# Optimization experiments

Hardware: AMD Instinct MI355X
Metric: run time of the kernel (lower is better)

The kernel has to match this reference:

```python
import jax, jax.numpy as jnp
import numpy as np

B, A, G = 256, 64, 978          # batch, n_atoms, num_gene
D_DRUG, D_CELL, D_DOSE = 128, 50, 128
CELL_IN, DOSE_IN = 978, 12
GLOBAL = D_DRUG + D_CELL + D_DOSE   # 306
EXP_IN = GLOBAL + 128               # 434
E, TOP_K = 4, 2


def setup_inputs() -> dict:
    key = jax.random.key(0)
    ks = jax.random.split(key, 24)
    w = lambda k, s: jax.random.normal(k, s, jnp.float32) * 0.05
    return {
        "drug_atom_embed": jax.random.normal(ks[0], (B, A, D_DRUG), jnp.float32),
        "input_cell_gex": jax.random.normal(ks[1], (B, CELL_IN), jnp.float32),
        "input_pert_idose": jax.random.normal(ks[2], (B, DOSE_IN), jnp.float32),
        # LinearEncoder: 978 -> 200 -> 100 -> 50 (ReLU after each)
        "cell_W1": w(ks[3], (CELL_IN, 200)), "cell_b1": jnp.zeros((200,), jnp.float32),
        "cell_W2": w(ks[4], (200, 100)),     "cell_b2": jnp.zeros((100,), jnp.float32),
        "cell_W3": w(ks[5], (100, D_CELL)),  "cell_b3": jnp.zeros((D_CELL,), jnp.float32),
        # DoseEncoder: 12 -> 64 -> 128 (ReLU after each; dropout off at eval)
        "dose_W1": w(ks[6], (DOSE_IN, 64)),  "dose_b1": jnp.zeros((64,), jnp.float32),
        "dose_W2": w(ks[7], (64, D_DOSE)),   "dose_b2": jnp.zeros((D_DOSE,), jnp.float32),
        # gene index embedding [num_gene, 128]
        "gene_emb": w(ks[8], (G, 128)),
        # GatingNetwork: 306 -> 128 -> 4
        "gate_W1": w(ks[9], (GLOBAL, 128)),  "gate_b1": jnp.zeros((128,), jnp.float32),
        "gate_W2": w(ks[10], (128, E)),      "gate_b2": jnp.zeros((E,), jnp.float32),
        # 4 ExpertNetworks stacked: 434 -> 128 -> 1
        "exp_W1": w(ks[11], (E, EXP_IN, 128)), "exp_b1": jnp.zeros((E, 128), jnp.float32),
        "exp_W2": w(ks[12], (E, 128, 1)),      "exp_b2": jnp.zeros((E, 1), jnp.float32),
    }


def reference(drug_atom_embed, input_cell_gex, input_pert_idose,
              cell_W1, cell_b1, cell_W2, cell_b2, cell_W3, cell_b3,
              dose_W1, dose_b1, dose_W2, dose_b2, gene_emb,
              gate_W1, gate_b1, gate_W2, gate_b2,
              exp_W1, exp_b1, exp_W2, exp_b2):
    relu = jax.nn.relu
    # drug: sum atom embeddings -> [B, 128]
    drug = drug_atom_embed.sum(axis=1)
    # cell encoder -> [B, 50]
    cell = relu(input_cell_gex @ cell_W1 + cell_b1)
    cell = relu(cell @ cell_W2 + cell_b2)
    cell = relu(cell @ cell_W3 + cell_b3)
    # dose encoder -> [B, 128]
    dose = relu(input_pert_idose @ dose_W1 + dose_b1)
    dose = relu(dose @ dose_W2 + dose_b2)
    # global features [B, 306]
    g = jnp.concatenate([drug, cell, dose], axis=1)
    # gating: top-k sparse gates [B, E]
    logits = relu(g @ gate_W1 + gate_b1) @ gate_W2 + gate_b2
    top_v, top_i = jax.lax.top_k(logits, TOP_K)
    top_g = jax.nn.softmax(top_v, axis=1)
    gates = jnp.zeros_like(logits).at[jnp.arange(logits.shape[0])[:, None], top_i].set(top_g)
    # gene-aware expert input [B, G, 434]
    expert_input = jnp.concatenate([
        jnp.broadcast_to(g[:, None, :], (g.shape[0], G, GLOBAL)),
        jnp.broadcast_to(gene_emb[None, :, :], (g.shape[0], G, 128)),
    ], axis=2)
    # all experts: [B, E, G, 128] -> [B, E, G]
    h = relu(jnp.einsum('bgi,eih->begh', expert_input, exp_W1) + exp_b1[None, :, None, :])
    o = jnp.einsum('begh,eho->beg', h, exp_W2) + exp_b2[None, :, :1]  # exp_b2[e,0] broadcast
    predictions = jnp.einsum('beg,be->bg', o, gates)
    return predictions, cell
```

## Files before the change

### kernel.cpp

```cpp
#include <hip/hip_runtime.h>

#define NB 256
#define NA 64
#define NG 978
#define CELL_IN 978
#define DOSE_IN 12
#define GLOBAL_F 306
#define EXP_IN 434
#define NE 4

#define WS_SEL 0
#define WS_U   (WS_SEL + NB*4)
#define WS_V   (WS_U + NB*256)

#define A_BLOCKS 256
#define AB_GRID  (NB + A_BLOCKS)

__device__ __forceinline__ float wave_reduce(float p) {
    #pragma unroll
    for (int off = 32; off > 0; off >>= 1) p += __shfl_down(p, off, 64);
    return p;
}

__global__ __launch_bounds__(1024) void ab_kernel(
    const float* __restrict__ drug, const float* __restrict__ gex,
    const float* __restrict__ idose,
    const float* __restrict__ cW1, const float* __restrict__ cb1,
    const float* __restrict__ cW2, const float* __restrict__ cb2,
    const float* __restrict__ cW3, const float* __restrict__ cb3,
    const float* __restrict__ dW1, const float* __restrict__ db1,
    const float* __restrict__ dW2, const float* __restrict__ db2,
    const float* __restrict__ gW1, const float* __restrict__ gb1,
    const float* __restrict__ gW2, const float* __restrict__ gb2,
    const float* __restrict__ eW1, const float* __restrict__ eb1,
    const float* __restrict__ gene,
    float* __restrict__ ws, float* __restrict__ cell_out)
{
    __shared__ float s_gex[CELL_IN];
    __shared__ float s_g[GLOBAL_F];
    __shared__ float s_h1[200];
    __shared__ float s_h2[100];
    __shared__ float s_gh[128];
    __shared__ float s_d1[64];
    __shared__ int   s_isel[2];
    __shared__ float s_part[16 * 200];
    __shared__ float s_pu[32 * 128];
    __shared__ float s_gene[64 * 129];

    const int blk = blockIdx.x, tid = threadIdx.x;

    if (blk >= NB) {
        const int ablk = blk - NB;
        const int tile = ablk >> 4, e = (ablk >> 2) & 3, hq = ablk & 3;

        for (int i = tid; i < 64 * 128; i += 1024) {
            int gl = i >> 7, k = i & 127;
            int g = tile * 64 + gl;
            s_gene[gl * 129 + k] = (g < NG) ? gene[g * 128 + k] : 0.f;
        }
        __syncthreads();

        const int slice = tid >> 6, g_in = tid & 63;
        const int h0 = hq * 32 + slice * 2;
        const float* wbase = eW1 + ((size_t)e * EXP_IN + GLOBAL_F) * 128 + h0;
        float a0 = 0.f, a1 = 0.f;
        #pragma unroll 8
        for (int k = 0; k < 128; ++k) {
            float x = s_gene[g_in * 129 + k];
            float2 w = *(const float2*)(wbase + (size_t)k * 128);
            a0 += x * w.x; a1 += x * w.y;
        }
        float* vout = ws + WS_V + ((size_t)tile * 512 + e * 128 + h0) * 64 + g_in;
        vout[0]  = a0;
        vout[64] = a1;
        return;
    }

    const int b = blk;

    if (tid < CELL_IN) s_gex[tid] = gex[b * CELL_IN + tid];
    {
        int row = tid >> 7, d = tid & 127;
        const float* p = drug + ((size_t)b * NA) * 128 + d;
        float acc = 0.f;
        #pragma unroll
        for (int i = 0; i < 8; ++i) acc += p[(size_t)(i * 8 + row) * 128];
        s_pu[row * 128 + d] = acc;
    }
    __syncthreads();
    if (tid < 128) {
        float a = 0.f;
        #pragma unroll
        for (int r = 0; r < 8; ++r) a += s_pu[r * 128 + tid];
        s_g[tid] = a;
    } else if (tid < 192) {
        int j = tid - 128;
        float acc = db1[j];
        #pragma unroll
        for (int i = 0; i < DOSE_IN; ++i)
            acc += idose[b * DOSE_IN + i] * dW1[i * 64 + j];
        s_d1[j] = fmaxf(acc, 0.f);
    }
    __syncthreads();
    if (tid < 128) {
        float acc = db2[tid];
        #pragma unroll 8
        for (int i = 0; i < 64; ++i) acc += s_d1[i] * dW2[i * 128 + tid];
        s_g[178 + tid] = fmaxf(acc, 0.f);
    }
    __syncthreads();

    {
        int q = tid & 63, ks = tid >> 6;
        if (q < 50) {
            int i0 = ks * 62, i1 = min(i0 + 62, CELL_IN);
            float4 acc = {0.f, 0.f, 0.f, 0.f};
            #pragma unroll 4
            for (int i = i0; i < i1; ++i) {
                float4 w = *(const float4*)(cW1 + (size_t)i * 200 + 4 * q);
                float x = s_gex[i];
                acc.x += x * w.x; acc.y += x * w.y; acc.z += x * w.z; acc.w += x * w.w;
            }
            *(float4*)(&s_part[ks * 200 + 4 * q]) = acc;
        }
    }
    __syncthreads();
    if (tid < 200) {
        float a = cb1[tid];
        #pragma unroll
        for (int ks = 0; ks < 16; ++ks) a += s_part[ks * 200 + tid];
        s_h1[tid] = fmaxf(a, 0.f);
    }
    __syncthreads();

    {
        int q = tid & 31, ks = tid >> 5;
        if (q < 25 && ks < 16) {
            int i0 = ks * 13, i1 = min(i0 + 13, 200);
            float4 acc = {0.f, 0.f, 0.f, 0.f};
            #pragma unroll
            for (int i = i0; i < i1; ++i) {
                float4 w = *(const float4*)(cW2 + (size_t)i * 100 + 4 * q);
                float x = s_h1[i];
                acc.x += x * w.x; acc.y += x * w.y; acc.z += x * w.z; acc.w += x * w.w;
            }
            *(float4*)(&s_part[ks * 100 + 4 * q]) = acc;
        }
    }
    __syncthreads();
    if (tid < 100) {
        float a = cb2[tid];
        #pragma unroll
        for (int ks = 0; ks < 16; ++ks) a += s_part[ks * 100 + tid];
        s_h2[tid] = fmaxf(a, 0.f);
    }
    __syncthreads();

    {
        int j = tid & 63, ks = tid >> 6;
        if (j < 50 && ks < 8) {
            int i0 = ks * 13, i1 = min(i0 + 13, 100);
            float acc = 0.f;
            #pragma unroll
            for (int i = i0; i < i1; ++i) acc += s_h2[i] * cW3[i * 50 + j];
            s_part[ks * 64 + j] = acc;
        }
    }
    __syncthreads();
    if (tid < 50) {
        float a = cb3[tid];
        #pragma unroll
        for (int ks = 0; ks < 8; ++ks) a += s_part[ks * 64 + tid];
        float r = fmaxf(a, 0.f);
        s_g[128 + tid] = r;
        cell_out[b * 50 + tid] = r;
    }
    __syncthreads();

    {
        int q = tid & 31, ks = tid >> 5;
        if (ks < 16) {
            int i0 = ks * 20, i1 = min(i0 + 20, GLOBAL_F);
            float4 acc = {0.f, 0.f, 0.f, 0.f};
            #pragma unroll
            for (int i = i0; i < i1; ++i) {
                float4 w = *(const float4*)(gW1 + (size_t)i * 128 + 4 * q);
                float x = s_g[i];
                acc.x += x * w.x; acc.y += x * w.y; acc.z += x * w.z; acc.w += x * w.w;
            }
            *(float4*)(&s_part[ks * 128 + 4 * q]) = acc;
        }
    }
    __syncthreads();
    if (tid < 128) {
        float a = gb1[tid];
        #pragma unroll
        for (int ks = 0; ks < 16; ++ks) a += s_part[ks * 128 + tid];
        s_gh[tid] = fmaxf(a, 0.f);
    }
    __syncthreads();

    if (tid < 64) {
        float h0 = s_gh[tid], h1 = s_gh[tid + 64];
        float logit[NE];
        #pragma unroll
        for (int j = 0; j < NE; ++j) {
            float p = h0 * gW2[tid * NE + j] + h1 * gW2[(tid + 64) * NE + j];
            p = wave_reduce(p);
            logit[j] = p + gb2[j];
        }
        if (tid == 0) {
            int i1 = 0; float v1 = logit[0];
            #pragma unroll
            for (int i = 1; i < NE; ++i) if (logit[i] > v1) { v1 = logit[i]; i1 = i; }
            int i2 = -1; float v2 = -__builtin_inff();
            #pragma unroll
            for (int i = 0; i < NE; ++i) {
                if (i == i1) continue;
                if (logit[i] > v2) { v2 = logit[i]; i2 = i; }
            }
            float ex = __expf(v2 - v1);
            float inv = 1.f / (1.f + ex);
            s_isel[0] = i1; s_isel[1] = i2;
            ws[WS_SEL + b * 4 + 0] = (float)i1;
            ws[WS_SEL + b * 4 + 1] = (float)i2;
            ws[WS_SEL + b * 4 + 2] = inv;
            ws[WS_SEL + b * 4 + 3] = ex * inv;
        }
    }
    __syncthreads();

    {
        int es = tid >> 9, ks = (tid >> 5) & 15, h4 = tid & 31;
        int e = s_isel[es];
        int i0 = ks * 20, i1 = min(i0 + 20, GLOBAL_F);
        const float* wp = eW1 + (size_t)e * EXP_IN * 128 + 4 * h4;
        float4 acc = {0.f, 0.f, 0.f, 0.f};
        #pragma unroll
        for (int i = i0; i < i1; ++i) {
            float4 w = *(const float4*)(wp + (size_t)i * 128);
            float x = s_g[i];
            acc.x += x * w.x; acc.y += x * w.y; acc.z += x * w.z; acc.w += x * w.w;
        }
        *(float4*)(&s_pu[(es * 16 + ks) * 128 + 4 * h4]) = acc;
    }
    __syncthreads();
    if (tid < 256) {
        int es = tid >> 7, h = tid & 127;
        int e = s_isel[es];
        float a = eb1[e * 128 + h];
        #pragma unroll
        for (int ks = 0; ks < 16; ++ks) a += s_pu[(es * 16 + ks) * 128 + h];
        ws[WS_U + (size_t)b * 256 + es * 128 + h] = a;
    }
}

__global__ __launch_bounds__(256) void c_kernel(
    const float* __restrict__ eW2, const float* __restrict__ eb2,
    const float* __restrict__ ws, float* __restrict__ pred)
{
    __shared__ float s_u[256];
    __shared__ float s_w2[256];
    const int b = blockIdx.x >> 2, quad = blockIdx.x & 3, tid = threadIdx.x;

    const int ea = (int)ws[WS_SEL + b * 4 + 0];
    const int eb = (int)ws[WS_SEL + b * 4 + 1];
    const float gA = ws[WS_SEL + b * 4 + 2];
    const float gB = ws[WS_SEL + b * 4 + 3];
    const float bA = eb2[ea], bB = eb2[eb];

    s_u[tid] = ws[WS_U + (size_t)b * 256 + tid];
    s_w2[tid] = (tid < 128) ? eW2[ea * 128 + tid] : eW2[eb * 128 + (tid - 128)];
    __syncthreads();

    const int wv = tid >> 6, lane = tid & 63;
    const int tile = quad * 4 + wv;
    const float* vA = ws + WS_V + ((size_t)tile * 512 + ea * 128) * 64 + lane;
    const float* vB = ws + WS_V + ((size_t)tile * 512 + eb * 128) * 64 + lane;

    float dA = 0.f, dB = 0.f;
    #pragma unroll 8
    for (int h = 0; h < 128; ++h) {
        dA += fmaxf(s_u[h]       + vA[(size_t)h * 64], 0.f) * s_w2[h];
        dB += fmaxf(s_u[128 + h] + vB[(size_t)h * 64], 0.f) * s_w2[128 + h];
    }
    const int g = tile * 64 + lane;
    if (g < NG) pred[(size_t)b * NG + g] = gA * (dA + bA) + gB * (dB + bB);
}

extern "C" void kernel_launch(void* const* d_in, const int* in_sizes, int n_in,
                              void* d_out, int out_size, void* d_ws, size_t ws_size,
                              hipStream_t stream) {
    const float* drug  = (const float*)d_in[0];
    const float* gex   = (const float*)d_in[1];
    const float* idose = (const float*)d_in[2];
    const float* cW1 = (const float*)d_in[3];  const float* cb1 = (const float*)d_in[4];
    const float* cW2 = (const float*)d_in[5];  const float* cb2 = (const float*)d_in[6];
    const float* cW3 = (const float*)d_in[7];  const float* cb3 = (const float*)d_in[8];
    const float* dW1 = (const float*)d_in[9];  const float* db1 = (const float*)d_in[10];
    const float* dW2 = (const float*)d_in[11]; const float* db2 = (const float*)d_in[12];
    const float* gene = (const float*)d_in[13];
    const float* gW1 = (const float*)d_in[14]; const float* gb1 = (const float*)d_in[15];
    const float* gW2 = (const float*)d_in[16]; const float* gb2 = (const float*)d_in[17];
    const float* eW1 = (const float*)d_in[18]; const float* eb1 = (const float*)d_in[19];
    const float* eW2 = (const float*)d_in[20]; const float* eb2 = (const float*)d_in[21];

    float* ws   = (float*)d_ws;
    float* out  = (float*)d_out;
    float* pred = out;
    float* cell = out + NB * NG;

    ab_kernel<<<AB_GRID, 1024, 0, stream>>>(drug, gex, idose,
        cW1, cb1, cW2, cb2, cW3, cb3, dW1, db1, dW2, db2,
        gW1, gb1, gW2, gb2, eW1, eb1, gene, ws, cell);
    c_kernel<<<NB * 4, 256, 0, stream>>>(eW2, eb2, ws, pred);
}
```

Before: 150.3 us.

## Vectorize V layout to float4 and split K across block halves

The gene-projection blocks now give each thread four hidden units over half of the K range. The two halves are reduced through shared memory, and results are written in a float4-interleaved V layout. The combine kernel reads V, U and W2 as float4 directly from global memory instead of staging them in shared memory. It also uses readfirstlane to keep the selected experts and gates scalar. This aims to cut load instruction count and the shared-memory staging barrier, at the cost of an extra sync and a reduction step in the projection blocks.

```diff
diff --git a/kernel.cpp b/kernel.cpp
--- a/kernel.cpp
+++ b/kernel.cpp
@@ -20,6 +20,10 @@
     #pragma unroll
     for (int off = 32; off > 0; off >>= 1) p += __shfl_down(p, off, 64);
     return p;
+}
+
+__device__ __forceinline__ float rfl(float x) {
+    return __int_as_float(__builtin_amdgcn_readfirstlane(__float_as_int(x)));
 }
 
 __global__ __launch_bounds__(1024) void ab_kernel(
@@ -60,19 +64,30 @@
         }
         __syncthreads();
 
-        const int slice = tid >> 6, g_in = tid & 63;
-        const int h0 = hq * 32 + slice * 2;
-        const float* wbase = eW1 + ((size_t)e * EXP_IN + GLOBAL_F) * 128 + h0;
-        float a0 = 0.f, a1 = 0.f;
+        const int g_in  = tid & 63;
+        const int slice = (tid >> 6) & 7;
+        const int khalf = tid >> 9;
+        const int h0 = hq * 32 + slice * 4;
+        const float* wbase = eW1
+            + ((size_t)e * EXP_IN + GLOBAL_F + khalf * 64) * 128 + h0;
+        float4 acc = {0.f, 0.f, 0.f, 0.f};
         #pragma unroll 8
-        for (int k = 0; k < 128; ++k) {
-            float x = s_gene[g_in * 129 + k];
-            float2 w = *(const float2*)(wbase + (size_t)k * 128);
-            a0 += x * w.x; a1 += x * w.y;
-        }
-        float* vout = ws + WS_V + ((size_t)tile * 512 + e * 128 + h0) * 64 + g_in;
-        vout[0]  = a0;
-        vout[64] = a1;
+        for (int k = 0; k < 64; ++k) {
+            float x = s_gene[g_in * 129 + khalf * 64 + k];
+            float4 w = *(const float4*)(wbase + (size_t)k * 128);
+            acc.x += x * w.x; acc.y += x * w.y; acc.z += x * w.z; acc.w += x * w.w;
+        }
+        *(float4*)&s_pu[(khalf * 512 + slice * 64 + g_in) * 4] = acc;
+        __syncthreads();
+        if (khalf == 0) {
+            float4 a0 = *(const float4*)&s_pu[(slice * 64 + g_in) * 4];
+            float4 a1 = *(const float4*)&s_pu[(512 + slice * 64 + g_in) * 4];
+            float4 r = {a0.x + a1.x, a0.y + a1.y, a0.z + a1.z, a0.w + a1.w};
+            const int q = hq * 8 + slice;
+            float* vout = ws + WS_V
+                + ((size_t)(tile * 4 + e)) * 8192 + q * 256 + g_in * 4;
+            *(float4*)vout = r;
+        }
         return;
     }
 
@@ -259,30 +274,37 @@
     const float* __restrict__ eW2, const float* __restrict__ eb2,
     const float* __restrict__ ws, float* __restrict__ pred)
 {
-    __shared__ float s_u[256];
-    __shared__ float s_w2[256];
     const int b = blockIdx.x >> 2, quad = blockIdx.x & 3, tid = threadIdx.x;
 
-    const int ea = (int)ws[WS_SEL + b * 4 + 0];
-    const int eb = (int)ws[WS_SEL + b * 4 + 1];
-    const float gA = ws[WS_SEL + b * 4 + 2];
-    const float gB = ws[WS_SEL + b * 4 + 3];
+    const float* sel = ws + WS_SEL + (size_t)b * 4;
+    const int ea = __builtin_amdgcn_readfirstlane((int)sel[0]);
+    const int eb = __builtin_amdgcn_readfirstlane((int)sel[1]);
+    const float gA = rfl(sel[2]);
+    const float gB = rfl(sel[3]);
     const float bA = eb2[ea], bB = eb2[eb];
 
-    s_u[tid] = ws[WS_U + (size_t)b * 256 + tid];
-    s_w2[tid] = (tid < 128) ? eW2[ea * 128 + tid] : eW2[eb * 128 + (tid - 128)];
-    __syncthreads();
+    const float* pu = ws + WS_U + (size_t)b * 256;
+    const float* wA = eW2 + ea * 128;
+    const float* wB = eW2 + eb * 128;
 
     const int wv = tid >> 6, lane = tid & 63;
     const int tile = quad * 4 + wv;
-    const float* vA = ws + WS_V + ((size_t)tile * 512 + ea * 128) * 64 + lane;
-    const float* vB = ws + WS_V + ((size_t)tile * 512 + eb * 128) * 64 + lane;
+    const float* vA = ws + WS_V + ((size_t)(tile * 4 + ea)) * 8192 + lane * 4;
+    const float* vB = ws + WS_V + ((size_t)(tile * 4 + eb)) * 8192 + lane * 4;
 
     float dA = 0.f, dB = 0.f;
     #pragma unroll 8
-    for (int h = 0; h < 128; ++h) {
-        dA += fmaxf(s_u[h]       + vA[(size_t)h * 64], 0.f) * s_w2[h];
-        dB += fmaxf(s_u[128 + h] + vB[(size_t)h * 64], 0.f) * s_w2[128 + h];
+    for (int q = 0; q < 32; ++q) {
+        float4 va = *(const float4*)(vA + q * 256);
+        float4 ua = *(const float4*)(pu + q * 4);
+        float4 wa = *(const float4*)(wA + q * 4);
+        dA += fmaxf(ua.x + va.x, 0.f) * wa.x + fmaxf(ua.y + va.y, 0.f) * wa.y
+            + fmaxf(ua.z + va.z, 0.f) * wa.z + fmaxf(ua.w + va.w, 0.f) * wa.w;
+        float4 vb = *(const float4*)(vB + q * 256);
+        float4 ub = *(const float4*)(pu + 128 + q * 4);
+        float4 wb = *(const float4*)(wB + q * 4);
+        dB += fmaxf(ub.x + vb.x, 0.f) * wb.x + fmaxf(ub.y + vb.y, 0.f) * wb.y
+            + fmaxf(ub.z + vb.z, 0.f) * wb.z + fmaxf(ub.w + vb.w, 0.f) * wb.w;
     }
     const int g = tile * 64 + lane;
     if (g < NG) pred[(size_t)b * NG + g] = gA * (dA + bA) + gB * (dB + bB);
```

After: 153.5 us. 2.1% more time.
